# Kernel tuning notes

Measured on AMD Instinct MI355X. Metric: run time of the kernel, lower is better.

Reference implementation:

```python
import jax, jax.numpy as jnp
import numpy as np
import math

B, T, D = 2, 2048, 1024
H = 16
HD = D // H
DFF = 4096
EPS = 1e-5


def setup_inputs() -> dict:
    key = jax.random.key(0)
    ks = jax.random.split(key, 11)
    s = 0.02
    return {
        "x": jax.random.normal(ks[0], (B, T, D), dtype=jnp.float32),
        "scale1": jnp.ones((D,), jnp.float32),
        "scale2": jnp.ones((D,), jnp.float32),
        "Wqkv": jax.random.normal(ks[1], (D, 3 * D), jnp.float32) * s,
        "bqkv": jnp.zeros((3 * D,), jnp.float32),
        "Wo": jax.random.normal(ks[2], (D, D), jnp.float32) * s,
        "bo": jnp.zeros((D,), jnp.float32),
        "W1": jax.random.normal(ks[3], (D, DFF), jnp.float32) * s,
        "b1": jnp.zeros((DFF,), jnp.float32),
        "W2": jax.random.normal(ks[4], (DFF, D), jnp.float32) * s,
        "b2": jnp.zeros((D,), jnp.float32),
    }


def rmsnorm(x, scale):
    # Faithful to source: norm = ||x||/sqrt(d); out = scale * x / (norm + eps)
    d = x.shape[-1]
    norm = jnp.linalg.norm(x, axis=-1, keepdims=True) * (1.0 / math.sqrt(d))
    return scale * x / (norm + EPS)


def attention(x, Wqkv, bqkv, Wo, bo):
    b, t, c = x.shape
    qkv = x @ Wqkv + bqkv                       # [B,T,3D]
    qkv = qkv.reshape(b, t, 3, H, HD)
    q, k, v = qkv[:, :, 0], qkv[:, :, 1], qkv[:, :, 2]   # [B,T,H,HD]
    scores = jnp.einsum("bqhd,bkhd->bhqk", q, k) / math.sqrt(HD)
    w = jax.nn.softmax(scores, axis=-1)
    out = jnp.einsum("bhqk,bkhd->bqhd", w, v).reshape(b, t, c)
    return out @ Wo + bo


def reference(x, scale1, scale2, Wqkv, bqkv, Wo, bo, W1, b1, W2, b2):
    x = x + attention(rmsnorm(x, scale1), Wqkv, bqkv, Wo, bo)
    h = rmsnorm(x, scale2)
    ff = (jax.nn.gelu(h @ W1 + b1, approximate=False)) @ W2 + b2
    return x + ff
```

## Files before the change

### kernel.cpp

```cpp
#include <hip/hip_runtime.h>
#include <hip/hip_bf16.h>
#include <math.h>

typedef unsigned short u16;
typedef __bf16 bf16x8 __attribute__((ext_vector_type(8)));
typedef float f32x4 __attribute__((ext_vector_type(4)));
typedef unsigned int u32x2 __attribute__((ext_vector_type(2)));

#define B_   2
#define T_   2048
#define D_   1024
#define H_   16
#define HD_  64
#define DFF_ 4096
#define M_TOK (B_*T_)

__device__ __forceinline__ u16 f2bf(float f){
  unsigned u = __float_as_uint(f);
  u += 0x7fff + ((u>>16)&1);
  return (u16)(u>>16);
}
__device__ __forceinline__ float bflo(unsigned u){ return __uint_as_float(u<<16); }
__device__ __forceinline__ float bfhi(unsigned u){ return __uint_as_float(u & 0xffff0000u); }

__device__ __forceinline__ void gl2lds16(const void* g, void* l){
  __builtin_amdgcn_global_load_lds((const __attribute__((address_space(1))) void*)g,
                                   (__attribute__((address_space(3))) void*)l, 16, 0, 0);
}

__device__ __forceinline__ unsigned lds_u32(const void* p){
  return (unsigned)(uintptr_t)(const __attribute__((address_space(3))) void*)p;
}

__device__ __forceinline__ u32x2 tr_read(unsigned addr){
  u32x2 d;
  asm volatile("ds_read_b64_tr_b16 %0, %1" : "=v"(d) : "v"(addr));
  return d;
}
__device__ __forceinline__ u32x2 tr_read512(unsigned addr){
  u32x2 d;
  asm volatile("ds_read_b64_tr_b16 %0, %1 offset:512" : "=v"(d) : "v"(addr));
  return d;
}
__device__ __forceinline__ bf16x8 pack8(u32x2 a, u32x2 b){
  union { u32x2 u[2]; bf16x8 v; } x; x.u[0]=a; x.u[1]=b; return x.v;
}
__device__ __forceinline__ unsigned cvt_pk_bf16(float a, float b){
  unsigned r;
  asm("v_cvt_pk_bf16_f32 %0, %1, %2" : "=v"(r) : "v"(a), "v"(b));
  return r;
}

__device__ __forceinline__ void block_barrier(){
  asm volatile("" ::: "memory");
  __builtin_amdgcn_s_barrier();
  __builtin_amdgcn_sched_barrier(0);
  asm volatile("" ::: "memory");
}

__device__ __forceinline__ int xcd_chunk(int orig, int nwg){
  int q = nwg >> 3, r = nwg & 7;
  int x = orig & 7, s = orig >> 3;
  return (x < r ? x*(q+1) : r*(q+1) + (x-r)*q) + s;
}

__global__ __launch_bounds__(256) void k_transpose_bf16(const float* __restrict__ in,
                                                        u16* __restrict__ out, int K, int N){
  __shared__ float t[32][33];
  int bx = blockIdx.x*32, by = blockIdx.y*32;
  int tx = threadIdx.x, ty = threadIdx.y;
  #pragma unroll
  for(int i=ty;i<32;i+=8) t[i][tx] = in[(size_t)(by+i)*N + bx + tx];
  __syncthreads();
  #pragma unroll
  for(int i=ty;i<32;i+=8) out[(size_t)(bx+i)*K + by + tx] = f2bf(t[tx][i]);
}

__global__ __launch_bounds__(256) void k_rmsnorm_bf16(const float* __restrict__ x,
                                                      const float* __restrict__ scale,
                                                      u16* __restrict__ out){
  int row = blockIdx.x;
  int tid = threadIdx.x;
  int lane = tid&63, wave = tid>>6;
  const float4* xr = (const float4*)(x + (size_t)row*D_);
  float4 v = xr[tid];
  float ss = v.x*v.x + v.y*v.y + v.z*v.z + v.w*v.w;
  #pragma unroll
  for(int o=1;o<64;o<<=1) ss += __shfl_xor(ss, o);
  __shared__ float red[4];
  if(lane==0) red[wave]=ss;
  __syncthreads();
  float tot = red[0]+red[1]+red[2]+red[3];
  float inv = 1.0f/(sqrtf(tot*(1.0f/D_)) + 1e-5f);
  const float4* sr = (const float4*)scale;
  float4 s4 = sr[tid];
  u16* o4 = out + (size_t)row*D_ + tid*4;
  o4[0]=f2bf(v.x*s4.x*inv); o4[1]=f2bf(v.y*s4.y*inv);
  o4[2]=f2bf(v.z*s4.z*inv); o4[3]=f2bf(v.w*s4.w*inv);
}

template<int EPI>
__global__ __launch_bounds__(512,2) void k_gemm256(const u16* __restrict__ A, const u16* __restrict__ Bt,
                                                   const float* __restrict__ bias,
                                                   void* __restrict__ Cout, int M, int N, int K,
                                                   int nbx, int nby, int splitk){
  __shared__ u16 LDS[4][16384];
  const int tid = threadIdx.x;
  const int lane = tid&63, wave = tid>>6;
  const int lo = lane&15, hi = lane>>4;
  const int wm = wave>>2, wn = wave&3;
  const int l = xcd_chunk(blockIdx.x, gridDim.x);
  const int row0 = (l % nbx)*256;
  const int col0 = ((l / nbx) % nby)*256;
  const int kc   = l / (nbx*nby);
  const int klen = K/splitk, kbeg = kc*klen;
  f32x4 acc[8][4];
  #pragma unroll
  for(int m=0;m<8;m++)
    #pragma unroll
    for(int n=0;n<4;n++) acc[m][n] = (f32x4){0.f,0.f,0.f,0.f};
  const u16* Ag = A + (size_t)row0*K + kbeg;
  const u16* Bg = Bt + (size_t)col0*K + kbeg;
  const int NT = klen>>5;

  const int cc0 = tid, cc1 = tid+512;
  const size_t s0 = (size_t)(cc0>>2)*K + (size_t)((((cc0&3)^((cc0>>3)&3)))<<3);
  const size_t s1 = (size_t)(cc1>>2)*K + (size_t)((((cc1&3)^((cc1>>3)&3)))<<3);

  #define STAGE_A(t) { const u16* Ab = Ag + (size_t)(t)*32; char* d = (char*)LDS[(t)&3]; \
    gl2lds16(Ab + s0, d + cc0*16); gl2lds16(Ab + s1, d + cc1*16); }
  #define STAGE_B(t) { const u16* Bb = Bg + (size_t)(t)*32; char* d = (char*)LDS[(t)&3] + 16384; \
    gl2lds16(Bb + s0, d + cc0*16); gl2lds16(Bb + s1, d + cc1*16); }

  STAGE_A(0); STAGE_B(0); STAGE_A(1); STAGE_B(1); STAGE_A(2); STAGE_B(2);

  const unsigned slot = (unsigned)((hi ^ ((lo>>1)&3))<<4);
  for(int t=0;t<NT;t++){
    if(t<NT-2)       { asm volatile("s_waitcnt vmcnt(8)" ::: "memory"); }
    else if(t==NT-2) { asm volatile("s_waitcnt vmcnt(4)" ::: "memory"); }
    else             { asm volatile("s_waitcnt vmcnt(0)" ::: "memory"); }
    block_barrier();
    const char* bufp = (const char*)LDS[t&3];
    const char* ap = bufp + (wm*128 + lo)*64 + slot;
    const char* bp = bufp + 16384 + (wn*64 + lo)*64 + slot;

    if(t+3<NT) STAGE_A(t+3);
    __builtin_amdgcn_sched_barrier(0);
    bf16x8 a0[4], b[4];
    #pragma unroll
    for(int m=0;m<4;m++) a0[m] = *(const bf16x8*)(ap + m*1024);
    #pragma unroll
    for(int n=0;n<4;n++) b[n]  = *(const bf16x8*)(bp + n*1024);
    __builtin_amdgcn_s_setprio(1);
    #pragma unroll
    for(int m=0;m<4;m++)
      #pragma unroll
      for(int n=0;n<4;n++)
        acc[m][n] = __builtin_amdgcn_mfma_f32_16x16x32_bf16(a0[m], b[n], acc[m][n], 0,0,0);
    __builtin_amdgcn_s_setprio(0);

    if(t+3<NT) STAGE_B(t+3);
    __builtin_amdgcn_sched_barrier(0);
    bf16x8 a1[4];
    #pragma unroll
    for(int m=0;m<4;m++) a1[m] = *(const bf16x8*)(ap + 4096 + m*1024);
    __builtin_amdgcn_s_setprio(1);
    #pragma unroll
    for(int m=0;m<4;m++)
      #pragma unroll
      for(int n=0;n<4;n++)
        acc[m+4][n] = __builtin_amdgcn_mfma_f32_16x16x32_bf16(a1[m], b[n], acc[m+4][n], 0,0,0);
    __builtin_amdgcn_s_setprio(0);
  }
  #undef STAGE_A
  #undef STAGE_B

  u16* Pk = (u16*)Cout + (size_t)kc*M*N;
  #pragma unroll
  for(int m=0;m<8;m++){
    #pragma unroll
    for(int n=0;n<4;n++){
      #pragma unroll
      for(int r=0;r<4;r++){
        int row = row0 + wm*128 + m*16 + hi*4 + r;
        int col = col0 + wn*64 + n*16 + lo;
        if constexpr(EPI==3){
          Pk[(size_t)row*N + col] = f2bf(acc[m][n][r]);
        } else {
          float v = acc[m][n][r] + bias[col];
          if constexpr(EPI==2){
            v = 0.5f*v*(1.0f + erff(v*0.70710678118f));
          }
          ((u16*)Cout)[(size_t)row*N + col] = f2bf(v);
        }
      }
    }
  }
}

__global__ __launch_bounds__(256) void k_ff2_reduce4(const u16* __restrict__ P,
                                                     const float* __restrict__ bias,
                                                     const float* __restrict__ res,
                                                     float* __restrict__ out){
  const size_t stride8 = (size_t)M_TOK*D_/8;
  size_t idx = (size_t)blockIdx.x*256 + threadIdx.x;
  const uint4* p = (const uint4*)P;
  uint4 q0 = p[idx], q1 = p[idx+stride8], q2 = p[idx+2*stride8], q3 = p[idx+3*stride8];
  size_t base = idx*8;
  const float4* rr = (const float4*)(res + base);
  const float4* bb = (const float4*)(bias + (base & (D_-1)));
  float4 r0 = rr[0], r1 = rr[1];
  float4 b0 = bb[0], b1 = bb[1];
  float4 o0, o1;
  unsigned w;
  w=q0.x; o0.x  = bflo(w); o0.y  = bfhi(w);
  w=q0.y; o0.z  = bflo(w); o0.w  = bfhi(w);
  w=q0.z; o1.x  = bflo(w); o1.y  = bfhi(w);
  w=q0.w; o1.z  = bflo(w); o1.w  = bfhi(w);
  w=q1.x; o0.x += bflo(w); o0.y += bfhi(w);
  w=q1.y; o0.z += bflo(w); o0.w += bfhi(w);
  w=q1.z; o1.x += bflo(w); o1.y += bfhi(w);
  w=q1.w; o1.z += bflo(w); o1.w += bfhi(w);
  w=q2.x; o0.x += bflo(w); o0.y += bfhi(w);
  w=q2.y; o0.z += bflo(w); o0.w += bfhi(w);
  w=q2.z; o1.x += bflo(w); o1.y += bfhi(w);
  w=q2.w; o1.z += bflo(w); o1.w += bfhi(w);
  w=q3.x; o0.x += bflo(w); o0.y += bfhi(w);
  w=q3.y; o0.z += bflo(w); o0.w += bfhi(w);
  w=q3.z; o1.x += bflo(w); o1.y += bfhi(w);
  w=q3.w; o1.z += bflo(w); o1.w += bfhi(w);
  o0.x += b0.x + r0.x; o0.y += b0.y + r0.y; o0.z += b0.z + r0.z; o0.w += b0.w + r0.w;
  o1.x += b1.x + r1.x; o1.y += b1.y + r1.y; o1.z += b1.z + r1.z; o1.w += b1.w + r1.w;
  float4* oo = (float4*)(out + base);
  oo[0] = o0; oo[1] = o1;
}

__global__ __launch_bounds__(256) void k_wo_reduce_rms(const u16* __restrict__ P,
                                                       const float* __restrict__ bo,
                                                       const float* __restrict__ x,
                                                       const float* __restrict__ scale2,
                                                       float* __restrict__ x2,
                                                       u16* __restrict__ xn2){
  int row = blockIdx.x;
  int tid = threadIdx.x;
  int lane = tid&63, wave = tid>>6;
  const size_t stride = (size_t)M_TOK*D_;
  const u16* pr = P + (size_t)row*D_;
  uint2 a0 = ((const uint2*)pr)[tid];
  uint2 a1 = ((const uint2*)(pr + stride))[tid];
  uint2 a2 = ((const uint2*)(pr + 2*stride))[tid];
  uint2 a3 = ((const uint2*)(pr + 3*stride))[tid];
  float4 r = ((const float4*)(x + (size_t)row*D_))[tid];
  float4 bi = ((const float4*)bo)[tid];
  float4 v;
  v.x = bflo(a0.x)+bflo(a1.x)+bflo(a2.x)+bflo(a3.x) + bi.x + r.x;
  v.y = bfhi(a0.x)+bfhi(a1.x)+bfhi(a2.x)+bfhi(a3.x) + bi.y + r.y;
  v.z = bflo(a0.y)+bflo(a1.y)+bflo(a2.y)+bflo(a3.y) + bi.z + r.z;
  v.w = bfhi(a0.y)+bfhi(a1.y)+bfhi(a2.y)+bfhi(a3.y) + bi.w + r.w;
  ((float4*)(x2 + (size_t)row*D_))[tid] = v;
  float ss = v.x*v.x + v.y*v.y + v.z*v.z + v.w*v.w;
  #pragma unroll
  for(int o=1;o<64;o<<=1) ss += __shfl_xor(ss, o);
  __shared__ float red[4];
  if(lane==0) red[wave]=ss;
  __syncthreads();
  float tot = red[0]+red[1]+red[2]+red[3];
  float inv = 1.0f/(sqrtf(tot*(1.0f/D_)) + 1e-5f);
  float4 s4 = ((const float4*)scale2)[tid];
  u16* o4 = xn2 + (size_t)row*D_ + tid*4;
  o4[0]=f2bf(v.x*s4.x*inv); o4[1]=f2bf(v.y*s4.y*inv);
  o4[2]=f2bf(v.z*s4.z*inv); o4[3]=f2bf(v.w*s4.w*inv);
}

__global__ __launch_bounds__(256,4) void k_attn(const u16* __restrict__ qkv, u16* __restrict__ O){
  __shared__ alignas(16) u16 Ks[2][4096];
  __shared__ alignas(16) u16 Vs[2][4096];
  __shared__ alignas(16) u16 Ps[4][1024];
  const int l = xcd_chunk(blockIdx.x, 1024);
  const int qt = l & 31, bh = l >> 5;
  const int h = bh & 15, b = bh >> 4;
  const int tid = threadIdx.x, lane = tid&63, wave = tid>>6;
  const int lo = lane&15, hi = lane>>4, l7 = lane&7;
  const u16* qkvB = qkv + (size_t)b*T_*3072;
  const int hoff = h*64;
  const float C2 = 0.18033688f;

  const int q0 = qt*64 + wave*16;
  const u16* qp = qkvB + (size_t)(q0+lo)*3072 + hoff + hi*8;
  bf16x8 aq0 = *(const bf16x8*)qp;
  bf16x8 aq1 = *(const bf16x8*)(qp+32);

  size_t sK[2], sV[2];
  {
    int cc[2] = {tid, tid+256};
    #pragma unroll
    for(int i=0;i<2;i++){
      int c = cc[i];
      sK[i] = (size_t)(c>>3)*3072 + 1024 + hoff + (((c&7)^((c>>3)&7))<<3);
      int kv = ((c>>5)<<2) + ((c>>1)&3);
      int d0 = (((c&31)>>3)<<4) | ((c&1)<<3);
      sV[i] = (size_t)kv*3072 + 2048 + hoff + d0;
    }
  }
  const unsigned kb0 = (unsigned)lo*128 + (unsigned)((hi^l7))*16;
  const unsigned kb1 = (unsigned)lo*128 + (unsigned)(((hi|4)^l7))*16;
  const unsigned vtr = (unsigned)hi*1024 + (unsigned)lo*2;
  const unsigned swzQ = (unsigned)(lo&7)<<4;

  f32x4 oac[4];
  #pragma unroll
  for(int n=0;n<4;n++) oac[n] = (f32x4){0.f,0.f,0.f,0.f};
  float mrow = -1e30f;
  float lsum = 0.f;

  {
    char* kd = (char*)Ks[0]; char* vd = (char*)Vs[0];
    gl2lds16(qkvB + sK[0], kd + tid*16);
    gl2lds16(qkvB + sK[1], kd + tid*16 + 4096);
    gl2lds16(qkvB + sV[0], vd + tid*16);
    gl2lds16(qkvB + sV[1], vd + tid*16 + 4096);
  }
  int buf = 0;
  for(int t=0;t<T_/64;t++){
    __syncthreads();
    if(t < T_/64-1){
      size_t koff = (size_t)(t+1)*64*3072;
      char* kd = (char*)Ks[buf^1]; char* vd = (char*)Vs[buf^1];
      gl2lds16(qkvB + koff + sK[0], kd + tid*16);
      gl2lds16(qkvB + koff + sK[1], kd + tid*16 + 4096);
      gl2lds16(qkvB + koff + sV[0], vd + tid*16);
      gl2lds16(qkvB + koff + sV[1], vd + tid*16 + 4096);
    }
    const char* K_ = (const char*)Ks[buf];
    u16* P_ = Ps[wave];

    f32x4 s[4];
    __builtin_amdgcn_s_setprio(1);
    #pragma unroll
    for(int n=0;n<4;n++){
      bf16x8 k0f = *(const bf16x8*)(K_ + n*2048 + kb0);
      bf16x8 k1f = *(const bf16x8*)(K_ + n*2048 + kb1);
      f32x4 z = (f32x4){0.f,0.f,0.f,0.f};
      z = __builtin_amdgcn_mfma_f32_16x16x32_bf16(k0f, aq0, z, 0,0,0);
      z = __builtin_amdgcn_mfma_f32_16x16x32_bf16(k1f, aq1, z, 0,0,0);
      s[n] = z;
    }
    __builtin_amdgcn_s_setprio(0);

    float mx = s[0][0];
    #pragma unroll
    for(int n=0;n<4;n++)
      #pragma unroll
      for(int r=0;r<4;r++) mx = fmaxf(mx, s[n][r]);

    if(!__all(mx <= mrow + 64.0f)){
      float mm = fmaxf(mx, __shfl_xor(mx,16));
      mm = fmaxf(mm, __shfl_xor(mm,32));
      float nm = fmaxf(mrow, mm);
      float alpha = exp2f((mrow - nm)*C2);
      mrow = nm;
      lsum *= alpha;
      float ar[4];
      #pragma unroll
      for(int r=0;r<4;r++) ar[r] = __shfl(alpha, hi*4 + r);
      #pragma unroll
      for(int n=0;n<4;n++)
        #pragma unroll
        for(int r=0;r<4;r++) oac[n][r] *= ar[r];
    }

    const float nmC2 = -mrow*C2;
    #pragma unroll
    for(int n=0;n<4;n++){
      float p0v = exp2f(fmaf(s[n][0], C2, nmC2));
      float p1v = exp2f(fmaf(s[n][1], C2, nmC2));
      float p2v = exp2f(fmaf(s[n][2], C2, nmC2));
      float p3v = exp2f(fmaf(s[n][3], C2, nmC2));
      lsum += (p0v+p1v)+(p2v+p3v);
      u32x2 pw;
      pw[0] = cvt_pk_bf16(p0v, p1v);
      pw[1] = cvt_pk_bf16(p2v, p3v);
      *(u32x2*)((char*)P_ + (unsigned)lo*128 + (((unsigned)(n*32 + hi*8)) ^ swzQ)) = pw;
    }

    const unsigned vsb = lds_u32(Vs[buf]);
    #pragma unroll
    for(int kk=0;kk<2;kk++){
      bf16x8 ap = *(const bf16x8*)((const char*)P_ + (kk==0 ? kb0 : kb1));
      u32x2 t0[4], t1[4];
      #pragma unroll
      for(int n=0;n<4;n++){
        unsigned a = vsb + vtr + (unsigned)kk*4096 + (unsigned)n*128;
        t0[n] = tr_read(a);
        t1[n] = tr_read512(a);
      }
      asm volatile("s_waitcnt lgkmcnt(0)" ::: "memory");
      __builtin_amdgcn_sched_barrier(0);
      __builtin_amdgcn_s_setprio(1);
      #pragma unroll
      for(int n=0;n<4;n++){
        bf16x8 bv = pack8(t0[n], t1[n]);
        oac[n] = __builtin_amdgcn_mfma_f32_16x16x32_bf16(ap, bv, oac[n], 0,0,0);
      }
      __builtin_amdgcn_s_setprio(0);
    }
    buf ^= 1;
  }

  lsum += __shfl_xor(lsum, 16);
  lsum += __shfl_xor(lsum, 32);
  float linv = 1.0f/lsum;
  float lr[4];
  #pragma unroll
  for(int r=0;r<4;r++) lr[r] = __shfl(linv, hi*4 + r);
  size_t obase = ((size_t)b*T_ + q0)*D_ + hoff;
  #pragma unroll
  for(int n=0;n<4;n++)
    #pragma unroll
    for(int r=0;r<4;r++)
      O[obase + (size_t)(hi*4+r)*D_ + n*16 + lo] = f2bf(oac[n][r]*lr[r]);
}

extern "C" void kernel_launch(void* const* d_in, const int* in_sizes, int n_in,
                              void* d_out, int out_size, void* d_ws, size_t ws_size,
                              hipStream_t stream){
  (void)in_sizes; (void)n_in; (void)out_size; (void)ws_size;
  const float* x      = (const float*)d_in[0];
  const float* scale1 = (const float*)d_in[1];
  const float* scale2 = (const float*)d_in[2];
  const float* Wqkv   = (const float*)d_in[3];
  const float* bqkv   = (const float*)d_in[4];
  const float* Wo     = (const float*)d_in[5];
  const float* bo     = (const float*)d_in[6];
  const float* W1     = (const float*)d_in[7];
  const float* b1     = (const float*)d_in[8];
  const float* W2     = (const float*)d_in[9];
  const float* b2     = (const float*)d_in[10];
  float* out = (float*)d_out;

  char* w = (char*)d_ws;
  u16* xn1   = (u16*)w;  w += (size_t)M_TOK*D_*2;
  u16* qkvb  = (u16*)w;  w += (size_t)M_TOK*3*D_*2;
  u16* Obuf  = (u16*)w;  w += (size_t)M_TOK*D_*2;
  float* x2  = (float*)w; w += (size_t)M_TOK*D_*4;
  u16* xn2   = (u16*)w;  w += (size_t)M_TOK*D_*2;
  u16* h1    = (u16*)w;  w += (size_t)M_TOK*DFF_*2;
  u16* Wqkvt = (u16*)w;  w += (size_t)3*D_*D_*2;
  u16* Wot   = (u16*)w;  w += (size_t)D_*D_*2;
  u16* W1t   = (u16*)w;  w += (size_t)D_*DFF_*2;
  u16* W2t   = (u16*)w;  w += (size_t)DFF_*D_*2;
  u16* wop = (u16*)d_ws;
  u16* pkb = (u16*)d_ws;

  dim3 tb(32,8);
  k_transpose_bf16<<<dim3(3*D_/32, D_/32), tb, 0, stream>>>(Wqkv, Wqkvt, D_, 3*D_);
  k_transpose_bf16<<<dim3(D_/32,   D_/32), tb, 0, stream>>>(Wo,   Wot,   D_, D_);
  k_transpose_bf16<<<dim3(DFF_/32, D_/32), tb, 0, stream>>>(W1,   W1t,   D_, DFF_);
  k_transpose_bf16<<<dim3(D_/32, DFF_/32), tb, 0, stream>>>(W2,   W2t,   DFF_, D_);

  k_rmsnorm_bf16<<<M_TOK, 256, 0, stream>>>(x, scale1, xn1);
  k_gemm256<0><<<192, 512, 0, stream>>>(xn1, Wqkvt, bqkv, qkvb, M_TOK, 3*D_, D_, M_TOK/256, 3*D_/256, 1);
  k_attn<<<1024, 256, 0, stream>>>(qkvb, Obuf);
  k_gemm256<3><<<256, 512, 0, stream>>>(Obuf, Wot, nullptr, wop, M_TOK, D_, D_, M_TOK/256, D_/256, 4);
  k_wo_reduce_rms<<<M_TOK, 256, 0, stream>>>(wop, bo, x, scale2, x2, xn2);
  k_gemm256<2><<<256, 512, 0, stream>>>(xn2, W1t, b1, h1, M_TOK, DFF_, D_, M_TOK/256, DFF_/256, 1);
  k_gemm256<3><<<256, 512, 0, stream>>>(h1, W2t, nullptr, pkb, M_TOK, D_, DFF_, M_TOK/256, D_/256, 4);
  k_ff2_reduce4<<<2048, 256, 0, stream>>>(pkb, b2, x2, out);
}
```

Baseline: 260.8 us.

## Compute softmax row sums with an MFMA against ones and halve the P buffer

The softmax denominator is no longer accumulated as a scalar per lane. An extra MFMA multiplies the bf16 P tile by a ones vector, so the row sums land in accumulator layout and the final cross-lane shuffles go away. P is now written and read in two halves, one per PV k-step, using a smaller swizzled LDS buffer. This interleaves exp work with the V transpose reads and reduces LDS use. The max reduction is also rewritten as a flatter tree. In exchange the sum is taken over bf16-rounded P values and each tile gets two extra MFMAs.

```diff
diff --git a/kernel.cpp b/kernel.cpp
--- a/kernel.cpp
+++ b/kernel.cpp
@@ -275,7 +275,7 @@
 __global__ __launch_bounds__(256,4) void k_attn(const u16* __restrict__ qkv, u16* __restrict__ O){
   __shared__ alignas(16) u16 Ks[2][4096];
   __shared__ alignas(16) u16 Vs[2][4096];
-  __shared__ alignas(16) u16 Ps[4][1024];
+  __shared__ alignas(16) u16 Ps[4][512];
   const int l = xcd_chunk(blockIdx.x, 1024);
   const int qt = l & 31, bh = l >> 5;
   const int h = bh & 15, b = bh >> 4;
@@ -305,13 +305,20 @@
   const unsigned kb0 = (unsigned)lo*128 + (unsigned)((hi^l7))*16;
   const unsigned kb1 = (unsigned)lo*128 + (unsigned)(((hi|4)^l7))*16;
   const unsigned vtr = (unsigned)hi*1024 + (unsigned)lo*2;
-  const unsigned swzQ = (unsigned)(lo&7)<<4;
+  const unsigned pswz = (unsigned)(lo&3)<<4;
+  const unsigned pwr  = (unsigned)lo*64;
+  const unsigned prd  = (unsigned)lo*64 + (((unsigned)hi<<4) ^ pswz);
+
+  bf16x8 ones;
+  { union { u16 u[8]; bf16x8 v; } c;
+    #pragma unroll
+    for(int i=0;i<8;i++) c.u[i]=0x3F80; ones=c.v; }
 
   f32x4 oac[4];
   #pragma unroll
   for(int n=0;n<4;n++) oac[n] = (f32x4){0.f,0.f,0.f,0.f};
+  f32x4 oacl = (f32x4){0.f,0.f,0.f,0.f};
   float mrow = -1e30f;
-  float lsum = 0.f;
 
   {
     char* kd = (char*)Ks[0]; char* vd = (char*)Vs[0];
@@ -332,7 +339,7 @@
       gl2lds16(qkvB + koff + sV[1], vd + tid*16 + 4096);
     }
     const char* K_ = (const char*)Ks[buf];
-    u16* P_ = Ps[wave];
+    char* P_ = (char*)Ps[wave];
 
     f32x4 s[4];
     __builtin_amdgcn_s_setprio(1);
@@ -347,11 +354,11 @@
     }
     __builtin_amdgcn_s_setprio(0);
 
-    float mx = s[0][0];
-    #pragma unroll
-    for(int n=0;n<4;n++)
-      #pragma unroll
-      for(int r=0;r<4;r++) mx = fmaxf(mx, s[n][r]);
+    float mx = fmaxf(fmaxf(s[0][0], s[0][1]), fmaxf(s[0][2], s[0][3]));
+    mx = fmaxf(fmaxf(mx, s[1][0]), fmaxf(s[1][1], s[1][2]));
+    mx = fmaxf(fmaxf(mx, s[1][3]), fmaxf(s[2][0], s[2][1]));
+    mx = fmaxf(fmaxf(mx, s[2][2]), fmaxf(s[2][3], s[3][0]));
+    mx = fmaxf(fmaxf(mx, s[3][1]), fmaxf(s[3][2], s[3][3]));
 
     if(!__all(mx <= mrow + 64.0f)){
       float mm = fmaxf(mx, __shfl_xor(mx,16));
@@ -359,7 +366,6 @@
       float nm = fmaxf(mrow, mm);
       float alpha = exp2f((mrow - nm)*C2);
       mrow = nm;
-      lsum *= alpha;
       float ar[4];
       #pragma unroll
       for(int r=0;r<4;r++) ar[r] = __shfl(alpha, hi*4 + r);
@@ -367,26 +373,26 @@
       for(int n=0;n<4;n++)
         #pragma unroll
         for(int r=0;r<4;r++) oac[n][r] *= ar[r];
+      #pragma unroll
+      for(int r=0;r<4;r++) oacl[r] *= ar[r];
     }
 
     const float nmC2 = -mrow*C2;
-    #pragma unroll
-    for(int n=0;n<4;n++){
-      float p0v = exp2f(fmaf(s[n][0], C2, nmC2));
-      float p1v = exp2f(fmaf(s[n][1], C2, nmC2));
-      float p2v = exp2f(fmaf(s[n][2], C2, nmC2));
-      float p3v = exp2f(fmaf(s[n][3], C2, nmC2));
-      lsum += (p0v+p1v)+(p2v+p3v);
-      u32x2 pw;
-      pw[0] = cvt_pk_bf16(p0v, p1v);
-      pw[1] = cvt_pk_bf16(p2v, p3v);
-      *(u32x2*)((char*)P_ + (unsigned)lo*128 + (((unsigned)(n*32 + hi*8)) ^ swzQ)) = pw;
-    }
-
     const unsigned vsb = lds_u32(Vs[buf]);
     #pragma unroll
     for(int kk=0;kk<2;kk++){
-      bf16x8 ap = *(const bf16x8*)((const char*)P_ + (kk==0 ? kb0 : kb1));
+      #pragma unroll
+      for(int n2=0;n2<2;n2++){
+        const int n = kk*2 + n2;
+        float p0v = exp2f(fmaf(s[n][0], C2, nmC2));
+        float p1v = exp2f(fmaf(s[n][1], C2, nmC2));
+        float p2v = exp2f(fmaf(s[n][2], C2, nmC2));
+        float p3v = exp2f(fmaf(s[n][3], C2, nmC2));
+        u32x2 pw;
+        pw[0] = cvt_pk_bf16(p0v, p1v);
+        pw[1] = cvt_pk_bf16(p2v, p3v);
+        *(u32x2*)(P_ + pwr + (((unsigned)(n2*32 + hi*8)) ^ pswz)) = pw;
+      }
       u32x2 t0[4], t1[4];
       #pragma unroll
       for(int n=0;n<4;n++){
@@ -394,6 +400,7 @@
         t0[n] = tr_read(a);
         t1[n] = tr_read512(a);
       }
+      bf16x8 ap = *(const bf16x8*)(P_ + prd);
       asm volatile("s_waitcnt lgkmcnt(0)" ::: "memory");
       __builtin_amdgcn_sched_barrier(0);
       __builtin_amdgcn_s_setprio(1);
@@ -402,17 +409,15 @@
         bf16x8 bv = pack8(t0[n], t1[n]);
         oac[n] = __builtin_amdgcn_mfma_f32_16x16x32_bf16(ap, bv, oac[n], 0,0,0);
       }
+      oacl = __builtin_amdgcn_mfma_f32_16x16x32_bf16(ap, ones, oacl, 0,0,0);
       __builtin_amdgcn_s_setprio(0);
     }
     buf ^= 1;
   }
 
-  lsum += __shfl_xor(lsum, 16);
-  lsum += __shfl_xor(lsum, 32);
-  float linv = 1.0f/lsum;
   float lr[4];
   #pragma unroll
-  for(int r=0;r<4;r++) lr[r] = __shfl(linv, hi*4 + r);
+  for(int r=0;r<4;r++) lr[r] = 1.0f/oacl[r];
   size_t obase = ((size_t)b*T_ + q0)*D_ + hoff;
   #pragma unroll
   for(int n=0;n<4;n++)
```

Result: no change. 265.0 us (+1.6%).
